# Kernel tuning notes

Measured on AMD Instinct MI355X. Metric: run time of the kernel, lower is better.

Reference implementation:

```python
import jax, jax.numpy as jnp
import numpy as np

N_NODES = 100000
N_EDGES = 1600000
D_IN = 128
D_HID = 128
SCALE = 1.8
EPS = 1e-12


def setup_inputs() -> dict:
    key = jax.random.key(0)
    ks = jax.random.split(key, 7)
    x = jax.random.normal(ks[0], (N_NODES, D_IN), dtype=jnp.float32)
    W1 = jax.random.normal(ks[1], (D_HID, D_IN), dtype=jnp.float32) * 0.05
    b1 = jax.random.normal(ks[2], (D_HID,), dtype=jnp.float32) * 0.05
    W2 = jax.random.normal(ks[3], (D_HID, D_HID), dtype=jnp.float32) * 0.05
    b2 = jax.random.normal(ks[4], (D_HID,), dtype=jnp.float32) * 0.05
    src = jax.random.randint(ks[5], (N_EDGES,), 0, N_NODES, dtype=jnp.int64 if jax.config.jax_enable_x64 else jnp.int32)
    dst = jax.random.randint(ks[6], (N_EDGES,), 0, N_NODES, dtype=jnp.int64 if jax.config.jax_enable_x64 else jnp.int32)
    return {"x": x, "W1": W1, "b1": b1, "W2": W2, "b2": b2, "src": src, "dst": dst}


def reference(x, W1, b1, W2, b2, src, dst):
    N = x.shape[0]
    ones = jnp.ones((src.shape[0],), dtype=x.dtype)
    # GraphConv norm='both' degree normalizers (clamped to >=1 as in DGL)
    deg_out = jnp.maximum(jnp.zeros((N,), x.dtype).at[src].add(ones), 1.0)
    deg_in = jnp.maximum(jnp.zeros((N,), x.dtype).at[dst].add(ones), 1.0)
    norm_out = jax.lax.rsqrt(deg_out)[:, None]  # [N,1]
    norm_in = jax.lax.rsqrt(deg_in)[:, None]    # [N,1]

    def layer(h, W, b):
        # torch.nn.Linear: h @ W.T + b
        h = jnp.einsum('nd,kd->nk', h, W) + b
        # F.normalize(h, dim=1) * 1.8
        nrm = jnp.sqrt(jnp.sum(h * h, axis=1, keepdims=True))
        h = h / jnp.maximum(nrm, EPS) * SCALE
        # GraphConv (weight=False, bias=False, norm='both'):
        # D_out^{-1/2} -> sparse aggregate -> D_in^{-1/2}
        h = h * norm_out
        agg = jax.ops.segment_sum(h[src], dst, num_segments=N)
        return agg * norm_in

    h = layer(x, W1, b1)
    h = layer(h, W2, b2)
    return h
```

## Files before the change

### kernel.cpp

```cpp
#include <hip/hip_runtime.h>
#include <cstdint>
#include <cstddef>

#define D 128
#define NSCALE 1.8f
#define NEPS 1e-12f
#define EPB 8192
#define NLO 512
#define SCAP 9216

typedef __attribute__((ext_vector_type(8))) short bf16x8;
typedef __attribute__((ext_vector_type(8))) unsigned short u16x8;
typedef __attribute__((ext_vector_type(4))) float f32x4;

__device__ __forceinline__ ushort bf16_rtn(float f) {
    uint32_t u = __float_as_uint(f);
    u = u + 0x7FFFu + ((u >> 16) & 1u);
    return (ushort)(u >> 16);
}

__device__ __forceinline__ float bf16_to_f(ushort u) {
    return __uint_as_float((uint32_t)u << 16);
}

__global__ __launch_bounds__(256) void hist_high_kernel(const int* __restrict__ src,
                                                        const int* __restrict__ dst,
                                                        int* __restrict__ Hd,
                                                        int* __restrict__ Hs, int ne) {
    __shared__ int hd[256], hs[256];
    int t = threadIdx.x, b = blockIdx.x;
    hd[t] = 0; hs[t] = 0;
    __syncthreads();
    int base = b * EPB, end = min(ne, base + EPB);
    for (int i = base + t; i < end; i += 256) {
        atomicAdd(&hd[dst[i] >> 9], 1);
        atomicAdd(&hs[src[i] >> 9], 1);
    }
    __syncthreads();
    Hd[b * 256 + t] = hd[t];
    Hs[b * 256 + t] = hs[t];
}

__global__ __launch_bounds__(256) void scan_cols_kernel(int* __restrict__ Hd,
                                                        int* __restrict__ Hs,
                                                        int* __restrict__ total_d,
                                                        int* __restrict__ total_s, int nbk) {
    __shared__ int s[256];
    int* H = blockIdx.y ? Hs : Hd;
    int* tot = blockIdx.y ? total_s : total_d;
    int v = blockIdx.x, t = threadIdx.x;
    int val = (t < nbk) ? H[t * 256 + v] : 0;
    s[t] = val;
    __syncthreads();
    #pragma unroll
    for (int off = 1; off < 256; off <<= 1) {
        int u = (t >= off) ? s[t - off] : 0;
        __syncthreads();
        s[t] += u;
        __syncthreads();
    }
    if (t < nbk) H[t * 256 + v] = s[t] - val;
    if (t == nbk - 1) tot[v] = s[t];
}

__global__ __launch_bounds__(256) void scan_tot_kernel(const int* __restrict__ total_d,
                                                       const int* __restrict__ total_s,
                                                       int* __restrict__ Bd,
                                                       int* __restrict__ Bs, int hb) {
    __shared__ int s[256];
    const int* tot = blockIdx.x ? total_s : total_d;
    int* B = blockIdx.x ? Bs : Bd;
    int t = threadIdx.x;
    int val = (t < hb) ? tot[t] : 0;
    s[t] = val;
    __syncthreads();
    #pragma unroll
    for (int off = 1; off < 256; off <<= 1) {
        int u = (t >= off) ? s[t - off] : 0;
        __syncthreads();
        s[t] += u;
        __syncthreads();
    }
    if (t <= hb) B[t] = s[t] - val;
}

__global__ __launch_bounds__(256) void scatter_high_kernel(const int* __restrict__ src,
                                                           const int* __restrict__ dst,
                                                           const int* __restrict__ Hd,
                                                           const int* __restrict__ Hs,
                                                           const int* __restrict__ Bd,
                                                           const int* __restrict__ Bs,
                                                           int2* __restrict__ sd_pair,
                                                           int* __restrict__ ss_src,
                                                           int ne, int hb) {
    __shared__ int cur_d[256], cur_s[256];
    int t = threadIdx.x, b = blockIdx.x;
    if (t < hb) {
        cur_d[t] = Bd[t] + Hd[b * 256 + t];
        cur_s[t] = Bs[t] + Hs[b * 256 + t];
    }
    __syncthreads();
    int base = b * EPB, end = min(ne, base + EPB);
    for (int i = base + t; i < end; i += 256) {
        int d = dst[i], s = src[i];
        int pd = atomicAdd(&cur_d[d >> 9], 1);
        sd_pair[pd] = make_int2(d, s);
        int ps = atomicAdd(&cur_s[s >> 9], 1);
        ss_src[ps] = s;
    }
}

__global__ __launch_bounds__(512) void bucket_sort_kernel(const int2* __restrict__ sd_pair,
                                                          const int* __restrict__ Bd,
                                                          int* __restrict__ offs,
                                                          int* __restrict__ cnt_dst,
                                                          float* __restrict__ norm_in,
                                                          int* __restrict__ ssrc, int N) {
    __shared__ int h[NLO], sc[NLO], cur[NLO];
    __shared__ int stage[SCAP];
    int t = threadIdx.x, v = blockIdx.x;
    int beg = Bd[v], end = Bd[v + 1];
    int m = end - beg;
    h[t] = 0;
    __syncthreads();
    for (int i = beg + t; i < end; i += 512) atomicAdd(&h[sd_pair[i].x & (NLO - 1)], 1);
    __syncthreads();
    int cnt = h[t];
    sc[t] = cnt;
    __syncthreads();
    #pragma unroll
    for (int off = 1; off < NLO; off <<= 1) {
        int u = (t >= off) ? sc[t - off] : 0;
        __syncthreads();
        sc[t] += u;
        __syncthreads();
    }
    int excl = sc[t] - cnt;
    int g = (v << 9) + t;
    if (g < N) {
        offs[g] = beg + excl;
        cnt_dst[g] = cnt;
        norm_in[g] = rsqrtf((float)max(cnt, 1));
    }
    if (m <= SCAP) {
        cur[t] = excl;
        __syncthreads();
        for (int i = beg + t; i < end; i += 512) {
            int2 p = sd_pair[i];
            int pos = atomicAdd(&cur[p.x & (NLO - 1)], 1);
            stage[pos] = p.y;
        }
        __syncthreads();
        for (int j = t; j < m; j += 512) ssrc[beg + j] = stage[j];
    } else {
        cur[t] = beg + excl;
        __syncthreads();
        for (int i = beg + t; i < end; i += 512) {
            int2 p = sd_pair[i];
            int pos = atomicAdd(&cur[p.x & (NLO - 1)], 1);
            ssrc[pos] = p.y;
        }
    }
}

__global__ __launch_bounds__(512) void bucket_hist_kernel(const int* __restrict__ ss_src,
                                                          const int* __restrict__ Bs,
                                                          float* __restrict__ norm_out, int N) {
    __shared__ int h[NLO];
    int t = threadIdx.x, v = blockIdx.x;
    int beg = Bs[v], end = Bs[v + 1];
    h[t] = 0;
    __syncthreads();
    for (int i = beg + t; i < end; i += 512) atomicAdd(&h[ss_src[i] & (NLO - 1)], 1);
    __syncthreads();
    int g = (v << 9) + t;
    if (g < N) norm_out[g] = rsqrtf((float)max(h[t], 1));
}

__global__ __launch_bounds__(256) void mlp_mfma_kernel(const float* __restrict__ X,
                                                       const float* __restrict__ W,
                                                       const float* __restrict__ b,
                                                       const float* __restrict__ post,
                                                       ushort* __restrict__ Abuf, int N) {
    __shared__ ushort Wf[128 * 128];

    const int t = threadIdx.x;
    const int wave = t >> 6;
    const int lane = t & 63;
    const int q = lane >> 4;
    const int l16 = lane & 15;

    #pragma unroll
    for (int it = 0; it < 8; ++it) {
        int f = t + 256 * it;
        int j = f >> 8;
        int p = (f >> 6) & 3;
        int ln = f & 63;
        int n = 16 * j + (ln & 15);
        int k0 = 32 * p + 8 * (ln >> 4);
        const float* srcp = W + n * D + k0;
        float4 a0 = *(const float4*)(srcp);
        float4 a1 = *(const float4*)(srcp + 4);
        bf16x8 v;
        v[0] = (short)bf16_rtn(a0.x); v[1] = (short)bf16_rtn(a0.y);
        v[2] = (short)bf16_rtn(a0.z); v[3] = (short)bf16_rtn(a0.w);
        v[4] = (short)bf16_rtn(a1.x); v[5] = (short)bf16_rtn(a1.y);
        v[6] = (short)bf16_rtn(a1.z); v[7] = (short)bf16_rtn(a1.w);
        ((bf16x8*)Wf)[f] = v;
    }

    const int r0 = blockIdx.x * 128 + wave * 32;
    bf16x8 ahi[2][4], alo[2][4];
    #pragma unroll
    for (int rt = 0; rt < 2; ++rt) {
        int row = r0 + rt * 16 + l16;
        bool ok = (row < N);
        const float* xr = X + (size_t)(ok ? row : 0) * D;
        #pragma unroll
        for (int p = 0; p < 4; ++p) {
            int k0 = 32 * p + 8 * q;
            float4 a0 = ok ? *(const float4*)(xr + k0)     : make_float4(0, 0, 0, 0);
            float4 a1 = ok ? *(const float4*)(xr + k0 + 4) : make_float4(0, 0, 0, 0);
            float fv[8] = {a0.x, a0.y, a0.z, a0.w, a1.x, a1.y, a1.z, a1.w};
            bf16x8 h, l;
            #pragma unroll
            for (int e = 0; e < 8; ++e) {
                uint32_t u = __float_as_uint(fv[e]);
                h[e] = (short)(u >> 16);
                float hf = __uint_as_float(u & 0xFFFF0000u);
                l[e] = (short)(__float_as_uint(fv[e] - hf) >> 16);
            }
            ahi[rt][p] = h;
            alo[rt][p] = l;
        }
    }

    __syncthreads();

    f32x4 acc[2][8];
    #pragma unroll
    for (int rt = 0; rt < 2; ++rt)
        #pragma unroll
        for (int j = 0; j < 8; ++j) acc[rt][j] = (f32x4){0.f, 0.f, 0.f, 0.f};

    #pragma unroll
    for (int j = 0; j < 8; ++j) {
        #pragma unroll
        for (int p = 0; p < 4; ++p) {
            bf16x8 bb = ((bf16x8*)Wf)[(j * 4 + p) * 64 + lane];
            acc[0][j] = __builtin_amdgcn_mfma_f32_16x16x32_bf16(ahi[0][p], bb, acc[0][j], 0, 0, 0);
            acc[0][j] = __builtin_amdgcn_mfma_f32_16x16x32_bf16(alo[0][p], bb, acc[0][j], 0, 0, 0);
            acc[1][j] = __builtin_amdgcn_mfma_f32_16x16x32_bf16(ahi[1][p], bb, acc[1][j], 0, 0, 0);
            acc[1][j] = __builtin_amdgcn_mfma_f32_16x16x32_bf16(alo[1][p], bb, acc[1][j], 0, 0, 0);
        }
    }

    float bias[8];
    #pragma unroll
    for (int j = 0; j < 8; ++j) bias[j] = b[16 * j + l16];

    #pragma unroll
    for (int rt = 0; rt < 2; ++rt) {
        float ss[4] = {0.f, 0.f, 0.f, 0.f};
        #pragma unroll
        for (int j = 0; j < 8; ++j)
            #pragma unroll
            for (int r = 0; r < 4; ++r) {
                float v = acc[rt][j][r] + bias[j];
                acc[rt][j][r] = v;
                ss[r] += v * v;
            }
        #pragma unroll
        for (int m = 1; m <= 8; m <<= 1)
            #pragma unroll
            for (int r = 0; r < 4; ++r) ss[r] += __shfl_xor(ss[r], m);

        #pragma unroll
        for (int r = 0; r < 4; ++r) {
            int row = r0 + rt * 16 + 4 * q + r;
            if (row < N) {
                float f = NSCALE / fmaxf(sqrtf(ss[r]), NEPS) * post[row];
                #pragma unroll
                for (int j = 0; j < 8; ++j)
                    Abuf[(size_t)row * D + 16 * j + l16] = bf16_rtn(acc[rt][j][r] * f);
            }
        }
    }
}

__global__ __launch_bounds__(256) void agg_kernel(const ushort* __restrict__ A,
                                                  const int* __restrict__ sorted_src,
                                                  const int* __restrict__ offs,
                                                  const int* __restrict__ cnt,
                                                  const float* __restrict__ norm_in,
                                                  float* __restrict__ out, int N) {
    int wave = threadIdx.x >> 6;
    int node = blockIdx.x * 4 + wave;
    if (node >= N) return;
    int lane = threadIdx.x & 63;
    int g = lane >> 4;
    int c = lane & 15;
    int beg = offs[node];
    int len = cnt[node];
    const ushort* Ac = A + c * 8;

    float acc[8] = {0.f, 0.f, 0.f, 0.f, 0.f, 0.f, 0.f, 0.f};
    int i = 0;
    for (; i + 16 <= len; i += 16) {
        int s0 = sorted_src[beg + i + g];
        int s1 = sorted_src[beg + i + 4 + g];
        int s2 = sorted_src[beg + i + 8 + g];
        int s3 = sorted_src[beg + i + 12 + g];
        u16x8 v0 = *(const u16x8*)(Ac + (size_t)s0 * D);
        u16x8 v1 = *(const u16x8*)(Ac + (size_t)s1 * D);
        u16x8 v2 = *(const u16x8*)(Ac + (size_t)s2 * D);
        u16x8 v3 = *(const u16x8*)(Ac + (size_t)s3 * D);
        #pragma unroll
        for (int e = 0; e < 8; ++e)
            acc[e] += (bf16_to_f(v0[e]) + bf16_to_f(v1[e])) +
                      (bf16_to_f(v2[e]) + bf16_to_f(v3[e]));
    }
    for (; i + 4 <= len; i += 4) {
        int s = sorted_src[beg + i + g];
        u16x8 v = *(const u16x8*)(Ac + (size_t)s * D);
        #pragma unroll
        for (int e = 0; e < 8; ++e) acc[e] += bf16_to_f(v[e]);
    }
    int rem = len - i;
    if (g < rem) {
        int s = sorted_src[beg + i + g];
        u16x8 v = *(const u16x8*)(Ac + (size_t)s * D);
        #pragma unroll
        for (int e = 0; e < 8; ++e) acc[e] += bf16_to_f(v[e]);
    }

    #pragma unroll
    for (int e = 0; e < 8; ++e) {
        acc[e] += __shfl_xor(acc[e], 16);
        acc[e] += __shfl_xor(acc[e], 32);
    }

    if (g == 0) {
        float sc = norm_in[node];
        float4 w0 = make_float4(acc[0] * sc, acc[1] * sc, acc[2] * sc, acc[3] * sc);
        float4 w1 = make_float4(acc[4] * sc, acc[5] * sc, acc[6] * sc, acc[7] * sc);
        float* op = out + (size_t)node * D + c * 8;
        *(float4*)(op) = w0;
        *(float4*)(op + 4) = w1;
    }
}


extern "C" void kernel_launch(void* const* d_in, const int* in_sizes, int n_in,
                              void* d_out, int out_size, void* d_ws, size_t ws_size,
                              hipStream_t stream) {
    const float* x  = (const float*)d_in[0];
    const float* W1 = (const float*)d_in[1];
    const float* b1 = (const float*)d_in[2];
    const float* W2 = (const float*)d_in[3];
    const float* b2 = (const float*)d_in[4];
    const int* src  = (const int*)d_in[5];
    const int* dst  = (const int*)d_in[6];
    float* out = (float*)d_out;

    const int N  = in_sizes[0] / D;
    const int NE = in_sizes[5];
    const int NBK = (NE + EPB - 1) / EPB;
    const int HB  = (N + NLO - 1) / NLO;

    char* w = (char*)d_ws;
    auto take = [&](size_t bytes) { char* p = w; w += (bytes + 255) & ~(size_t)255; return p; };
    int*    Hd       = (int*)take((size_t)NBK * 256 * 4);
    int*    Hs       = (int*)take((size_t)NBK * 256 * 4);
    int*    total_d  = (int*)take(256 * 4);
    int*    total_s  = (int*)take(256 * 4);
    int*    Bd       = (int*)take((size_t)(HB + 1) * 4);
    int*    Bs       = (int*)take((size_t)(HB + 1) * 4);
    int2*   sd_pair  = (int2*)take((size_t)NE * 8);
    int*    ss_src   = (int*)take((size_t)NE * 4);
    int*    ssrc     = (int*)take((size_t)NE * 4);
    int*    offs     = (int*)take((size_t)N * 4);
    int*    cnt_dst  = (int*)take((size_t)N * 4);
    float*  norm_in  = (float*)take((size_t)N * 4);
    float*  norm_out = (float*)take((size_t)N * 4);
    ushort* Abuf     = (ushort*)take((size_t)N * D * 2);

    hist_high_kernel<<<NBK, 256, 0, stream>>>(src, dst, Hd, Hs, NE);
    scan_cols_kernel<<<dim3(HB, 2), 256, 0, stream>>>(Hd, Hs, total_d, total_s, NBK);
    scan_tot_kernel<<<2, 256, 0, stream>>>(total_d, total_s, Bd, Bs, HB);
    scatter_high_kernel<<<NBK, 256, 0, stream>>>(src, dst, Hd, Hs, Bd, Bs,
                                                 sd_pair, ss_src, NE, HB);
    bucket_sort_kernel<<<HB, 512, 0, stream>>>(sd_pair, Bd, offs, cnt_dst,
                                               norm_in, ssrc, N);
    bucket_hist_kernel<<<HB, 512, 0, stream>>>(ss_src, Bs, norm_out, N);

    const int mlp_blocks = (N + 127) / 128;
    const int agg_blocks = (N + 3) / 4;

    mlp_mfma_kernel<<<mlp_blocks, 256, 0, stream>>>(x, W1, b1, norm_out, Abuf, N);
    agg_kernel<<<agg_blocks, 256, 0, stream>>>(Abuf, ssrc, offs, cnt_dst, norm_in, out, N);

    mlp_mfma_kernel<<<mlp_blocks, 256, 0, stream>>>(out, W2, b2, norm_out, Abuf, N);
    agg_kernel<<<agg_blocks, 256, 0, stream>>>(Abuf, ssrc, offs, cnt_dst, norm_in, out, N);
}
```

Before: 342.7 us.

## Compute source degrees with global atomics and pad gather with a zero row

Source out-degrees are now counted with global atomics into a per-node array, which drops the separate source-side bucket sort pass (scatter of ss_src, column scan and bucket histogram kernel); norm_out is computed inside the destination bucket sort. The aggregation loop gets a single 16-wide unrolled loop that clamps out-of-range edges to an extra all-zero row appended to Abuf, removing the tail loops. This trades global atomic contention on a random-index degree array, plus wasted zero-row loads for low-degree nodes, for fewer kernels and less memory traffic.

```diff
diff --git a/kernel.cpp b/kernel.cpp
--- a/kernel.cpp
+++ b/kernel.cpp
@@ -10,7 +10,6 @@
 #define SCAP 9216
 
 typedef __attribute__((ext_vector_type(8))) short bf16x8;
-typedef __attribute__((ext_vector_type(8))) unsigned short u16x8;
 typedef __attribute__((ext_vector_type(4))) float f32x4;
 
 __device__ __forceinline__ ushort bf16_rtn(float f) {
@@ -19,37 +18,36 @@
     return (ushort)(u >> 16);
 }
 
-__device__ __forceinline__ float bf16_to_f(ushort u) {
-    return __uint_as_float((uint32_t)u << 16);
+__device__ __forceinline__ float blo(uint32_t u) { return __uint_as_float(u << 16); }
+__device__ __forceinline__ float bhi(uint32_t u) { return __uint_as_float(u & 0xFFFF0000u); }
+
+__global__ __launch_bounds__(256) void zero_kernel(int* __restrict__ p, int n) {
+    int i = blockIdx.x * 256 + threadIdx.x;
+    if (i < n) p[i] = 0;
 }
 
 __global__ __launch_bounds__(256) void hist_high_kernel(const int* __restrict__ src,
                                                         const int* __restrict__ dst,
                                                         int* __restrict__ Hd,
-                                                        int* __restrict__ Hs, int ne) {
-    __shared__ int hd[256], hs[256];
+                                                        int* __restrict__ degS, int ne) {
+    __shared__ int hd[256];
     int t = threadIdx.x, b = blockIdx.x;
-    hd[t] = 0; hs[t] = 0;
+    hd[t] = 0;
     __syncthreads();
     int base = b * EPB, end = min(ne, base + EPB);
     for (int i = base + t; i < end; i += 256) {
         atomicAdd(&hd[dst[i] >> 9], 1);
-        atomicAdd(&hs[src[i] >> 9], 1);
+        atomicAdd(&degS[src[i]], 1);
     }
     __syncthreads();
     Hd[b * 256 + t] = hd[t];
-    Hs[b * 256 + t] = hs[t];
 }
 
 __global__ __launch_bounds__(256) void scan_cols_kernel(int* __restrict__ Hd,
-                                                        int* __restrict__ Hs,
-                                                        int* __restrict__ total_d,
-                                                        int* __restrict__ total_s, int nbk) {
+                                                        int* __restrict__ total_d, int nbk) {
     __shared__ int s[256];
-    int* H = blockIdx.y ? Hs : Hd;
-    int* tot = blockIdx.y ? total_s : total_d;
     int v = blockIdx.x, t = threadIdx.x;
-    int val = (t < nbk) ? H[t * 256 + v] : 0;
+    int val = (t < nbk) ? Hd[t * 256 + v] : 0;
     s[t] = val;
     __syncthreads();
     #pragma unroll
@@ -59,19 +57,15 @@
         s[t] += u;
         __syncthreads();
     }
-    if (t < nbk) H[t * 256 + v] = s[t] - val;
-    if (t == nbk - 1) tot[v] = s[t];
+    if (t < nbk) Hd[t * 256 + v] = s[t] - val;
+    if (t == nbk - 1) total_d[v] = s[t];
 }
 
 __global__ __launch_bounds__(256) void scan_tot_kernel(const int* __restrict__ total_d,
-                                                       const int* __restrict__ total_s,
-                                                       int* __restrict__ Bd,
-                                                       int* __restrict__ Bs, int hb) {
+                                                       int* __restrict__ Bd, int hb) {
     __shared__ int s[256];
-    const int* tot = blockIdx.x ? total_s : total_d;
-    int* B = blockIdx.x ? Bs : Bd;
     int t = threadIdx.x;
-    int val = (t < hb) ? tot[t] : 0;
+    int val = (t < hb) ? total_d[t] : 0;
     s[t] = val;
     __syncthreads();
     #pragma unroll
@@ -81,40 +75,34 @@
         s[t] += u;
         __syncthreads();
     }
-    if (t <= hb) B[t] = s[t] - val;
+    if (t <= hb) Bd[t] = s[t] - val;
 }
 
 __global__ __launch_bounds__(256) void scatter_high_kernel(const int* __restrict__ src,
                                                            const int* __restrict__ dst,
                                                            const int* __restrict__ Hd,
-                                                           const int* __restrict__ Hs,
                                                            const int* __restrict__ Bd,
-                                                           const int* __restrict__ Bs,
                                                            int2* __restrict__ sd_pair,
-                                                           int* __restrict__ ss_src,
                                                            int ne, int hb) {
-    __shared__ int cur_d[256], cur_s[256];
+    __shared__ int cur_d[256];
     int t = threadIdx.x, b = blockIdx.x;
-    if (t < hb) {
-        cur_d[t] = Bd[t] + Hd[b * 256 + t];
-        cur_s[t] = Bs[t] + Hs[b * 256 + t];
-    }
+    if (t < hb) cur_d[t] = Bd[t] + Hd[b * 256 + t];
     __syncthreads();
     int base = b * EPB, end = min(ne, base + EPB);
     for (int i = base + t; i < end; i += 256) {
         int d = dst[i], s = src[i];
         int pd = atomicAdd(&cur_d[d >> 9], 1);
         sd_pair[pd] = make_int2(d, s);
-        int ps = atomicAdd(&cur_s[s >> 9], 1);
-        ss_src[ps] = s;
     }
 }
 
 __global__ __launch_bounds__(512) void bucket_sort_kernel(const int2* __restrict__ sd_pair,
                                                           const int* __restrict__ Bd,
+                                                          const int* __restrict__ degS,
                                                           int* __restrict__ offs,
                                                           int* __restrict__ cnt_dst,
                                                           float* __restrict__ norm_in,
+                                                          float* __restrict__ norm_out,
                                                           int* __restrict__ ssrc, int N) {
     __shared__ int h[NLO], sc[NLO], cur[NLO];
     __shared__ int stage[SCAP];
@@ -141,6 +129,7 @@
         offs[g] = beg + excl;
         cnt_dst[g] = cnt;
         norm_in[g] = rsqrtf((float)max(cnt, 1));
+        norm_out[g] = rsqrtf((float)max(degS[g], 1));
     }
     if (m <= SCAP) {
         cur[t] = excl;
@@ -161,20 +150,6 @@
             ssrc[pos] = p.y;
         }
     }
-}
-
-__global__ __launch_bounds__(512) void bucket_hist_kernel(const int* __restrict__ ss_src,
-                                                          const int* __restrict__ Bs,
-                                                          float* __restrict__ norm_out, int N) {
-    __shared__ int h[NLO];
-    int t = threadIdx.x, v = blockIdx.x;
-    int beg = Bs[v], end = Bs[v + 1];
-    h[t] = 0;
-    __syncthreads();
-    for (int i = beg + t; i < end; i += 512) atomicAdd(&h[ss_src[i] & (NLO - 1)], 1);
-    __syncthreads();
-    int g = (v << 9) + t;
-    if (g < N) norm_out[g] = rsqrtf((float)max(h[t], 1));
 }
 
 __global__ __launch_bounds__(256) void mlp_mfma_kernel(const float* __restrict__ X,
@@ -189,6 +164,10 @@
     const int lane = t & 63;
     const int q = lane >> 4;
     const int l16 = lane & 15;
+
+    if (blockIdx.x == 0 && t < 16) {
+        ((uint4*)(Abuf + (size_t)N * D))[t] = make_uint4(0u, 0u, 0u, 0u);
+    }
 
     #pragma unroll
     for (int it = 0; it < 8; ++it) {
@@ -302,36 +281,30 @@
     int c = lane & 15;
     int beg = offs[node];
     int len = cnt[node];
+    int last = beg + len - 1;
     const ushort* Ac = A + c * 8;
 
     float acc[8] = {0.f, 0.f, 0.f, 0.f, 0.f, 0.f, 0.f, 0.f};
-    int i = 0;
-    for (; i + 16 <= len; i += 16) {
-        int s0 = sorted_src[beg + i + g];
-        int s1 = sorted_src[beg + i + 4 + g];
-        int s2 = sorted_src[beg + i + 8 + g];
-        int s3 = sorted_src[beg + i + 12 + g];
-        u16x8 v0 = *(const u16x8*)(Ac + (size_t)s0 * D);
-        u16x8 v1 = *(const u16x8*)(Ac + (size_t)s1 * D);
-        u16x8 v2 = *(const u16x8*)(Ac + (size_t)s2 * D);
-        u16x8 v3 = *(const u16x8*)(Ac + (size_t)s3 * D);
-        #pragma unroll
-        for (int e = 0; e < 8; ++e)
-            acc[e] += (bf16_to_f(v0[e]) + bf16_to_f(v1[e])) +
-                      (bf16_to_f(v2[e]) + bf16_to_f(v3[e]));
-    }
-    for (; i + 4 <= len; i += 4) {
-        int s = sorted_src[beg + i + g];
-        u16x8 v = *(const u16x8*)(Ac + (size_t)s * D);
-        #pragma unroll
-        for (int e = 0; e < 8; ++e) acc[e] += bf16_to_f(v[e]);
-    }
-    int rem = len - i;
-    if (g < rem) {
-        int s = sorted_src[beg + i + g];
-        u16x8 v = *(const u16x8*)(Ac + (size_t)s * D);
-        #pragma unroll
-        for (int e = 0; e < 8; ++e) acc[e] += bf16_to_f(v[e]);
+
+    for (int i = 0; i < len; i += 16) {
+        int e0 = beg + i + g;
+        int e1 = e0 + 4, e2 = e0 + 8, e3 = e0 + 12;
+        int s0 = sorted_src[min(e0, last)]; if (e0 > last) s0 = N;
+        int s1 = sorted_src[min(e1, last)]; if (e1 > last) s1 = N;
+        int s2 = sorted_src[min(e2, last)]; if (e2 > last) s2 = N;
+        int s3 = sorted_src[min(e3, last)]; if (e3 > last) s3 = N;
+        uint4 w0 = *(const uint4*)(Ac + (size_t)s0 * D);
+        uint4 w1 = *(const uint4*)(Ac + (size_t)s1 * D);
+        uint4 w2 = *(const uint4*)(Ac + (size_t)s2 * D);
+        uint4 w3 = *(const uint4*)(Ac + (size_t)s3 * D);
+        acc[0] += (blo(w0.x) + blo(w1.x)) + (blo(w2.x) + blo(w3.x));
+        acc[1] += (bhi(w0.x) + bhi(w1.x)) + (bhi(w2.x) + bhi(w3.x));
+        acc[2] += (blo(w0.y) + blo(w1.y)) + (blo(w2.y) + blo(w3.y));
+        acc[3] += (bhi(w0.y) + bhi(w1.y)) + (bhi(w2.y) + bhi(w3.y));
+        acc[4] += (blo(w0.z) + blo(w1.z)) + (blo(w2.z) + blo(w3.z));
+        acc[5] += (bhi(w0.z) + bhi(w1.z)) + (bhi(w2.z) + bhi(w3.z));
+        acc[6] += (blo(w0.w) + blo(w1.w)) + (blo(w2.w) + blo(w3.w));
+        acc[7] += (bhi(w0.w) + bhi(w1.w)) + (bhi(w2.w) + bhi(w3.w));
     }
 
     #pragma unroll
@@ -371,28 +344,24 @@
     char* w = (char*)d_ws;
     auto take = [&](size_t bytes) { char* p = w; w += (bytes + 255) & ~(size_t)255; return p; };
     int*    Hd       = (int*)take((size_t)NBK * 256 * 4);
-    int*    Hs       = (int*)take((size_t)NBK * 256 * 4);
     int*    total_d  = (int*)take(256 * 4);
-    int*    total_s  = (int*)take(256 * 4);
     int*    Bd       = (int*)take((size_t)(HB + 1) * 4);
-    int*    Bs       = (int*)take((size_t)(HB + 1) * 4);
+    int*    degS     = (int*)take((size_t)N * 4);
     int2*   sd_pair  = (int2*)take((size_t)NE * 8);
-    int*    ss_src   = (int*)take((size_t)NE * 4);
     int*    ssrc     = (int*)take((size_t)NE * 4);
     int*    offs     = (int*)take((size_t)N * 4);
     int*    cnt_dst  = (int*)take((size_t)N * 4);
     float*  norm_in  = (float*)take((size_t)N * 4);
     float*  norm_out = (float*)take((size_t)N * 4);
-    ushort* Abuf     = (ushort*)take((size_t)N * D * 2);
-
-    hist_high_kernel<<<NBK, 256, 0, stream>>>(src, dst, Hd, Hs, NE);
-    scan_cols_kernel<<<dim3(HB, 2), 256, 0, stream>>>(Hd, Hs, total_d, total_s, NBK);
-    scan_tot_kernel<<<2, 256, 0, stream>>>(total_d, total_s, Bd, Bs, HB);
-    scatter_high_kernel<<<NBK, 256, 0, stream>>>(src, dst, Hd, Hs, Bd, Bs,
-                                                 sd_pair, ss_src, NE, HB);
-    bucket_sort_kernel<<<HB, 512, 0, stream>>>(sd_pair, Bd, offs, cnt_dst,
-                                               norm_in, ssrc, N);
-    bucket_hist_kernel<<<HB, 512, 0, stream>>>(ss_src, Bs, norm_out, N);
+    ushort* Abuf     = (ushort*)take((size_t)(N + 1) * D * 2);
+
+    zero_kernel<<<(N + 255) / 256, 256, 0, stream>>>(degS, N);
+    hist_high_kernel<<<NBK, 256, 0, stream>>>(src, dst, Hd, degS, NE);
+    scan_cols_kernel<<<HB, 256, 0, stream>>>(Hd, total_d, NBK);
+    scan_tot_kernel<<<1, 256, 0, stream>>>(total_d, Bd, HB);
+    scatter_high_kernel<<<NBK, 256, 0, stream>>>(src, dst, Hd, Bd, sd_pair, NE, HB);
+    bucket_sort_kernel<<<HB, 512, 0, stream>>>(sd_pair, Bd, degS, offs, cnt_dst,
+                                               norm_in, norm_out, ssrc, N);
 
     const int mlp_blocks = (N + 127) / 128;
     const int agg_blocks = (N + 3) / 4;
```

Measured after the change: 378.0 us. 10.3% more time.

## Pack sort keys into 32-bit words and aggregate two nodes per wave

Applied to the files above, without the earlier changes.

The scatter step now packs the low destination bits and the source index into one 32-bit word, and stores the low source bits as 16-bit values. This cuts traffic for the intermediate sort buffers. The aggregation kernel now handles two destination nodes per wave with a fixed 8-way gather per iteration, sending out-of-range edges to a zeroed padding row at index N instead of using remainder loops. This raises memory-level parallelism but wastes loads when the two nodes' degrees differ, and the packing assumes node ids fit in 23 bits.

```diff
diff --git a/kernel.cpp b/kernel.cpp
--- a/kernel.cpp
+++ b/kernel.cpp
@@ -8,9 +8,10 @@
 #define EPB 8192
 #define NLO 512
 #define SCAP 9216
+#define SRCB 23
+#define SRCM 0x7FFFFF
 
 typedef __attribute__((ext_vector_type(8))) short bf16x8;
-typedef __attribute__((ext_vector_type(8))) unsigned short u16x8;
 typedef __attribute__((ext_vector_type(4))) float f32x4;
 
 __device__ __forceinline__ ushort bf16_rtn(float f) {
@@ -19,9 +20,8 @@
     return (ushort)(u >> 16);
 }
 
-__device__ __forceinline__ float bf16_to_f(ushort u) {
-    return __uint_as_float((uint32_t)u << 16);
-}
+__device__ __forceinline__ float blo(uint32_t u) { return __uint_as_float(u << 16); }
+__device__ __forceinline__ float bhi(uint32_t u) { return __uint_as_float(u & 0xFFFF0000u); }
 
 __global__ __launch_bounds__(256) void hist_high_kernel(const int* __restrict__ src,
                                                         const int* __restrict__ dst,
@@ -90,8 +90,8 @@
                                                            const int* __restrict__ Hs,
                                                            const int* __restrict__ Bd,
                                                            const int* __restrict__ Bs,
-                                                           int2* __restrict__ sd_pair,
-                                                           int* __restrict__ ss_src,
+                                                           uint32_t* __restrict__ spack,
+                                                           ushort* __restrict__ ss_low,
                                                            int ne, int hb) {
     __shared__ int cur_d[256], cur_s[256];
     int t = threadIdx.x, b = blockIdx.x;
@@ -104,13 +104,13 @@
     for (int i = base + t; i < end; i += 256) {
         int d = dst[i], s = src[i];
         int pd = atomicAdd(&cur_d[d >> 9], 1);
-        sd_pair[pd] = make_int2(d, s);
+        spack[pd] = ((uint32_t)(d & (NLO - 1)) << SRCB) | (uint32_t)s;
         int ps = atomicAdd(&cur_s[s >> 9], 1);
-        ss_src[ps] = s;
-    }
-}
-
-__global__ __launch_bounds__(512) void bucket_sort_kernel(const int2* __restrict__ sd_pair,
+        ss_low[ps] = (ushort)(s & (NLO - 1));
+    }
+}
+
+__global__ __launch_bounds__(512) void bucket_sort_kernel(const uint32_t* __restrict__ spack,
                                                           const int* __restrict__ Bd,
                                                           int* __restrict__ offs,
                                                           int* __restrict__ cnt_dst,
@@ -123,7 +123,7 @@
     int m = end - beg;
     h[t] = 0;
     __syncthreads();
-    for (int i = beg + t; i < end; i += 512) atomicAdd(&h[sd_pair[i].x & (NLO - 1)], 1);
+    for (int i = beg + t; i < end; i += 512) atomicAdd(&h[spack[i] >> SRCB], 1);
     __syncthreads();
     int cnt = h[t];
     sc[t] = cnt;
@@ -146,9 +146,9 @@
         cur[t] = excl;
         __syncthreads();
         for (int i = beg + t; i < end; i += 512) {
-            int2 p = sd_pair[i];
-            int pos = atomicAdd(&cur[p.x & (NLO - 1)], 1);
-            stage[pos] = p.y;
+            uint32_t p = spack[i];
+            int pos = atomicAdd(&cur[p >> SRCB], 1);
+            stage[pos] = (int)(p & SRCM);
         }
         __syncthreads();
         for (int j = t; j < m; j += 512) ssrc[beg + j] = stage[j];
@@ -156,14 +156,14 @@
         cur[t] = beg + excl;
         __syncthreads();
         for (int i = beg + t; i < end; i += 512) {
-            int2 p = sd_pair[i];
-            int pos = atomicAdd(&cur[p.x & (NLO - 1)], 1);
-            ssrc[pos] = p.y;
-        }
-    }
-}
-
-__global__ __launch_bounds__(512) void bucket_hist_kernel(const int* __restrict__ ss_src,
+            uint32_t p = spack[i];
+            int pos = atomicAdd(&cur[p >> SRCB], 1);
+            ssrc[pos] = (int)(p & SRCM);
+        }
+    }
+}
+
+__global__ __launch_bounds__(512) void bucket_hist_kernel(const ushort* __restrict__ ss_low,
                                                           const int* __restrict__ Bs,
                                                           float* __restrict__ norm_out, int N) {
     __shared__ int h[NLO];
@@ -171,7 +171,7 @@
     int beg = Bs[v], end = Bs[v + 1];
     h[t] = 0;
     __syncthreads();
-    for (int i = beg + t; i < end; i += 512) atomicAdd(&h[ss_src[i] & (NLO - 1)], 1);
+    for (int i = beg + t; i < end; i += 512) atomicAdd(&h[(int)ss_low[i]], 1);
     __syncthreads();
     int g = (v << 9) + t;
     if (g < N) norm_out[g] = rsqrtf((float)max(h[t], 1));
@@ -189,6 +189,10 @@
     const int lane = t & 63;
     const int q = lane >> 4;
     const int l16 = lane & 15;
+
+    if (blockIdx.x == 0 && t < 16) {
+        ((uint4*)(Abuf + (size_t)N * D))[t] = make_uint4(0u, 0u, 0u, 0u);
+    }
 
     #pragma unroll
     for (int it = 0; it < 8; ++it) {
@@ -295,58 +299,78 @@
                                                   const float* __restrict__ norm_in,
                                                   float* __restrict__ out, int N) {
     int wave = threadIdx.x >> 6;
-    int node = blockIdx.x * 4 + wave;
-    if (node >= N) return;
+    int n0 = (blockIdx.x * 4 + wave) * 2;
+    if (n0 >= N) return;
     int lane = threadIdx.x & 63;
     int g = lane >> 4;
     int c = lane & 15;
-    int beg = offs[node];
-    int len = cnt[node];
     const ushort* Ac = A + c * 8;
 
-    float acc[8] = {0.f, 0.f, 0.f, 0.f, 0.f, 0.f, 0.f, 0.f};
-    int i = 0;
-    for (; i + 16 <= len; i += 16) {
-        int s0 = sorted_src[beg + i + g];
-        int s1 = sorted_src[beg + i + 4 + g];
-        int s2 = sorted_src[beg + i + 8 + g];
-        int s3 = sorted_src[beg + i + 12 + g];
-        u16x8 v0 = *(const u16x8*)(Ac + (size_t)s0 * D);
-        u16x8 v1 = *(const u16x8*)(Ac + (size_t)s1 * D);
-        u16x8 v2 = *(const u16x8*)(Ac + (size_t)s2 * D);
-        u16x8 v3 = *(const u16x8*)(Ac + (size_t)s3 * D);
-        #pragma unroll
-        for (int e = 0; e < 8; ++e)
-            acc[e] += (bf16_to_f(v0[e]) + bf16_to_f(v1[e])) +
-                      (bf16_to_f(v2[e]) + bf16_to_f(v3[e]));
-    }
-    for (; i + 4 <= len; i += 4) {
-        int s = sorted_src[beg + i + g];
-        u16x8 v = *(const u16x8*)(Ac + (size_t)s * D);
-        #pragma unroll
-        for (int e = 0; e < 8; ++e) acc[e] += bf16_to_f(v[e]);
-    }
-    int rem = len - i;
-    if (g < rem) {
-        int s = sorted_src[beg + i + g];
-        u16x8 v = *(const u16x8*)(Ac + (size_t)s * D);
-        #pragma unroll
-        for (int e = 0; e < 8; ++e) acc[e] += bf16_to_f(v[e]);
+    int n1 = n0 + 1;
+    int beg0 = offs[n0], len0 = cnt[n0];
+    int beg1 = 0, len1 = 0;
+    if (n1 < N) { beg1 = offs[n1]; len1 = cnt[n1]; }
+    int last0 = beg0 + len0 - 1;
+    int last1 = beg1 + len1 - 1;
+
+    float a0[8] = {0.f, 0.f, 0.f, 0.f, 0.f, 0.f, 0.f, 0.f};
+    float a1[8] = {0.f, 0.f, 0.f, 0.f, 0.f, 0.f, 0.f, 0.f};
+
+    int mx = max(len0, len1);
+    for (int i = 0; i < mx; i += 16) {
+        int idx[8];
+        #pragma unroll
+        for (int k = 0; k < 4; ++k) {
+            int e = beg0 + i + g + 4 * k;
+            int cl = max(min(e, last0), 0);
+            idx[k] = sorted_src[cl];
+            if (e > last0) idx[k] = N;
+        }
+        #pragma unroll
+        for (int k = 0; k < 4; ++k) {
+            int e = beg1 + i + g + 4 * k;
+            int cl = max(min(e, last1), 0);
+            idx[4 + k] = sorted_src[cl];
+            if (e > last1) idx[4 + k] = N;
+        }
+        uint4 w[8];
+        #pragma unroll
+        for (int k = 0; k < 8; ++k) w[k] = *(const uint4*)(Ac + (size_t)idx[k] * D);
+        #pragma unroll
+        for (int k = 0; k < 4; ++k) {
+            a0[0] += blo(w[k].x); a0[1] += bhi(w[k].x);
+            a0[2] += blo(w[k].y); a0[3] += bhi(w[k].y);
+            a0[4] += blo(w[k].z); a0[5] += bhi(w[k].z);
+            a0[6] += blo(w[k].w); a0[7] += bhi(w[k].w);
+        }
+        #pragma unroll
+        for (int k = 4; k < 8; ++k) {
+            a1[0] += blo(w[k].x); a1[1] += bhi(w[k].x);
+            a1[2] += blo(w[k].y); a1[3] += bhi(w[k].y);
+            a1[4] += blo(w[k].z); a1[5] += bhi(w[k].z);
+            a1[6] += blo(w[k].w); a1[7] += bhi(w[k].w);
+        }
     }
 
     #pragma unroll
     for (int e = 0; e < 8; ++e) {
-        acc[e] += __shfl_xor(acc[e], 16);
-        acc[e] += __shfl_xor(acc[e], 32);
+        a0[e] += __shfl_xor(a0[e], 16);
+        a0[e] += __shfl_xor(a0[e], 32);
+        a1[e] += __shfl_xor(a1[e], 16);
+        a1[e] += __shfl_xor(a1[e], 32);
     }
 
     if (g == 0) {
-        float sc = norm_in[node];
-        float4 w0 = make_float4(acc[0] * sc, acc[1] * sc, acc[2] * sc, acc[3] * sc);
-        float4 w1 = make_float4(acc[4] * sc, acc[5] * sc, acc[6] * sc, acc[7] * sc);
-        float* op = out + (size_t)node * D + c * 8;
-        *(float4*)(op) = w0;
-        *(float4*)(op + 4) = w1;
+        float sc0 = norm_in[n0];
+        float* op0 = out + (size_t)n0 * D + c * 8;
+        *(float4*)(op0)     = make_float4(a0[0] * sc0, a0[1] * sc0, a0[2] * sc0, a0[3] * sc0);
+        *(float4*)(op0 + 4) = make_float4(a0[4] * sc0, a0[5] * sc0, a0[6] * sc0, a0[7] * sc0);
+        if (n1 < N) {
+            float sc1 = norm_in[n1];
+            float* op1 = out + (size_t)n1 * D + c * 8;
+            *(float4*)(op1)     = make_float4(a1[0] * sc1, a1[1] * sc1, a1[2] * sc1, a1[3] * sc1);
+            *(float4*)(op1 + 4) = make_float4(a1[4] * sc1, a1[5] * sc1, a1[6] * sc1, a1[7] * sc1);
+        }
     }
 }
 
@@ -370,32 +394,31 @@
 
     char* w = (char*)d_ws;
     auto take = [&](size_t bytes) { char* p = w; w += (bytes + 255) & ~(size_t)255; return p; };
-    int*    Hd       = (int*)take((size_t)NBK * 256 * 4);
-    int*    Hs       = (int*)take((size_t)NBK * 256 * 4);
-    int*    total_d  = (int*)take(256 * 4);
-    int*    total_s  = (int*)take(256 * 4);
-    int*    Bd       = (int*)take((size_t)(HB + 1) * 4);
-    int*    Bs       = (int*)take((size_t)(HB + 1) * 4);
-    int2*   sd_pair  = (int2*)take((size_t)NE * 8);
-    int*    ss_src   = (int*)take((size_t)NE * 4);
-    int*    ssrc     = (int*)take((size_t)NE * 4);
-    int*    offs     = (int*)take((size_t)N * 4);
-    int*    cnt_dst  = (int*)take((size_t)N * 4);
-    float*  norm_in  = (float*)take((size_t)N * 4);
-    float*  norm_out = (float*)take((size_t)N * 4);
-    ushort* Abuf     = (ushort*)take((size_t)N * D * 2);
+    int*      Hd       = (int*)take((size_t)NBK * 256 * 4);
+    int*      Hs       = (int*)take((size_t)NBK * 256 * 4);
+    int*      total_d  = (int*)take(256 * 4);
+    int*      total_s  = (int*)take(256 * 4);
+    int*      Bd       = (int*)take((size_t)(HB + 1) * 4);
+    int*      Bs       = (int*)take((size_t)(HB + 1) * 4);
+    uint32_t* spack    = (uint32_t*)take((size_t)NE * 4);
+    ushort*   ss_low   = (ushort*)take((size_t)NE * 2);
+    int*      ssrc     = (int*)take((size_t)NE * 4);
+    int*      offs     = (int*)take((size_t)N * 4);
+    int*      cnt_dst  = (int*)take((size_t)N * 4);
+    float*    norm_in  = (float*)take((size_t)N * 4);
+    float*    norm_out = (float*)take((size_t)N * 4);
+    ushort*   Abuf     = (ushort*)take((size_t)(N + 1) * D * 2);
 
     hist_high_kernel<<<NBK, 256, 0, stream>>>(src, dst, Hd, Hs, NE);
     scan_cols_kernel<<<dim3(HB, 2), 256, 0, stream>>>(Hd, Hs, total_d, total_s, NBK);
     scan_tot_kernel<<<2, 256, 0, stream>>>(total_d, total_s, Bd, Bs, HB);
     scatter_high_kernel<<<NBK, 256, 0, stream>>>(src, dst, Hd, Hs, Bd, Bs,
-                                                 sd_pair, ss_src, NE, HB);
-    bucket_sort_kernel<<<HB, 512, 0, stream>>>(sd_pair, Bd, offs, cnt_dst,
-                                               norm_in, ssrc, N);
-    bucket_hist_kernel<<<HB, 512, 0, stream>>>(ss_src, Bs, norm_out, N);
+                                                 spack, ss_low, NE, HB);
+    bucket_sort_kernel<<<HB, 512, 0, stream>>>(spack, Bd, offs, cnt_dst, norm_in, ssrc, N);
+    bucket_hist_kernel<<<HB, 512, 0, stream>>>(ss_low, Bs, norm_out, N);
 
     const int mlp_blocks = (N + 127) / 128;
-    const int agg_blocks = (N + 3) / 4;
+    const int agg_blocks = (N + 7) / 8;
 
     mlp_mfma_kernel<<<mlp_blocks, 256, 0, stream>>>(x, W1, b1, norm_out, Abuf, N);
     agg_kernel<<<agg_blocks, 256, 0, stream>>>(Abuf, ssrc, offs, cnt_dst, norm_in, out, N);
```

After: 335.5 us. -2.1%, faster.
